# Optimization experiments

Hardware: AMD Instinct MI355X
Metric: run time of the kernel (lower is better)

## Reference

```python
import itertools
import jax, jax.numpy as jnp
import numpy as np

# ---- config (mirrors args) ----
BS = 8; C = 20              # 4 + num_sem_categories
FH, FW = 480, 640           # frame height/width
DU = 2                      # du_scale
NSC = 16                    # num_sem_categories
RES = 5; ZRES = 5           # xy / z map resolution (cm)
MAP_CM = 4800 // 2          # map_size_cm // global_downscaling
VR = 100                    # vision_range
HFOV = 79.0
MAXH = int(200 / ZRES); MINH = int(-40 / ZRES)   # 40, -8
AGENT_H = 0.88 * 100.0
CAT_T, EXP_T, MAP_T = 5.0, 1.0, 1.0
STAIR_R = 30
DEG = 57.29577951308232
M = MAP_CM // RES           # 480 local map cells

CAM_XC = (FW - 1.) / 2.
CAM_ZC = (FH - 1.) / 2.
CAM_F = (FW / 2.) / np.tan(np.deg2rad(HFOV / 2.))
SHIFT_X = VR * RES // 2     # shift_loc theta = pi/2 -> identity rotation, +x only

def _circle_mask(r):
    size = 2 * r
    ii, jj = np.meshgrid(np.arange(size), np.arange(size), indexing='ij')
    return (((ii + 0.5 - size // 2) ** 2 + (jj + 0.5 - size // 2) ** 2) <= r ** 2).astype(np.float32)

CIRCLE = jnp.asarray(_circle_mask(STAIR_R))

def splat_feat_nd(init_grid, feat, coords):
    # init_grid [B,F,d0,d1,d2], feat [B,F,N], coords [B,3,N] in [-1,1]
    B, nF = init_grid.shape[:2]
    gd = init_grid.shape[2:]
    grid_flat = init_grid.reshape(B, nF, -1)
    pos_dim, wts_dim = [], []
    for d in range(3):
        pos = coords[:, d, :] * gd[d] / 2 + gd[d] / 2
        pd, wd = [], []
        for ix in (0, 1):
            pos_ix = jnp.floor(pos) + ix
            safe = ((pos_ix > 0) & (pos_ix < gd[d])).astype(pos.dtype)
            wd.append((1 - jnp.abs(pos - pos_ix)) * safe)
            pd.append(pos_ix * safe)
        pos_dim.append(pd); wts_dim.append(wd)
    idxs, vals = [], []
    for ix_d in itertools.product((0, 1), repeat=3):  # 8 trilinear corners
        index = jnp.zeros_like(pos_dim[0][0])
        wts = jnp.ones_like(wts_dim[0][0])
        for d in range(3):
            index = index * gd[d] + pos_dim[d][ix_d[d]]
            wts = wts * wts_dim[d][ix_d[d]]
        idxs.append(index.astype(jnp.int32))
        vals.append(feat * wts[:, None, :])
    idx = jnp.concatenate(idxs, -1)          # [B, 8N]
    val = jnp.concatenate(vals, -1)          # [B, F, 8N]
    grid_flat = jax.vmap(lambda g, i, v: g.at[:, i].add(v))(grid_flat, idx, val)
    return jnp.round(grid_flat).reshape(init_grid.shape)

def affine_grid(theta, H, W):
    # F.affine_grid, align_corners=False (torch default)
    xs = (jnp.arange(W, dtype=theta.dtype) + 0.5) * 2 / W - 1
    ys = (jnp.arange(H, dtype=theta.dtype) + 0.5) * 2 / H - 1
    gy, gx = jnp.meshgrid(ys, xs, indexing='ij')
    base = jnp.stack([gx, gy, jnp.ones_like(gx)], -1)   # [H,W,3]
    return jnp.einsum('bij,hwj->bhwi', theta, base)     # [B,H,W,2]

def grid_sample(img, grid):
    # bilinear, zero padding, align_corners=True
    B, C_, H, W = img.shape
    gx = (grid[..., 0] + 1.) * (W - 1) / 2.
    gy = (grid[..., 1] + 1.) * (H - 1) / 2.
    x0 = jnp.floor(gx); y0 = jnp.floor(gy)
    def gather(ix, iy):
        valid = ((ix >= 0) & (ix < W) & (iy >= 0) & (iy < H)).astype(img.dtype)
        ic = jnp.clip(ix, 0, W - 1).astype(jnp.int32)
        jc = jnp.clip(iy, 0, H - 1).astype(jnp.int32)
        v = jax.vmap(lambda im, yy, xx: im[:, yy, xx])(img, jc, ic)  # [B,C,H,W]
        return v * valid[:, None]
    wx1 = gx - x0; wx0 = 1 - wx1; wy1 = gy - y0; wy0 = 1 - wy1
    return (gather(x0, y0) * (wx0 * wy0)[:, None]
            + gather(x0 + 1, y0) * (wx1 * wy0)[:, None]
            + gather(x0, y0 + 1) * (wx0 * wy1)[:, None]
            + gather(x0 + 1, y0 + 1) * (wx1 * wy1)[:, None])

def maxpool3(x):
    return jax.lax.reduce_window(x, -jnp.inf, jax.lax.max,
                                 (1, 1, 3, 3), (1, 1, 1, 1),
                                 [(0, 0), (0, 0), (1, 1), (1, 1)])

def _forward(obs, pose_obs, maps_last, poses_last, eve_angle):
    bs, c, h, w = obs.shape
    hs, ws = h // DU, w // DU
    depth = obs[:, 3, ::DU, ::DU]
    # point cloud from depth (du.get_point_cloud_from_z_t)
    xg = jnp.arange(0, w, DU, dtype=obs.dtype)[None, None, :]
    zg = (h - 1 - jnp.arange(0, h, DU, dtype=obs.dtype))[None, :, None]
    X = (xg - CAM_XC) * depth / CAM_F
    Z = (zg - CAM_ZC) * depth / CAM_F
    # camera elevation rotation about x-axis (per-env eve_angle) + sensor height
    th = jnp.deg2rad(eve_angle)[:, None, None]
    ct, st = jnp.cos(th), jnp.sin(th)
    Yr = ct * depth - st * Z
    Zr = st * depth + ct * Z + AGENT_H
    Xs = X + SHIFT_X
    # normalize to [-1,1] voxel coords
    cx = (Xs / RES - VR // 2) / VR * 2.0
    cy = (Yr / RES - VR // 2) / VR * 2.0
    cz = (Zr / ZRES - (MAXH + MINH) // 2) / (MAXH - MINH) * 2.0
    coords = jnp.stack([cx.reshape(bs, -1), cy.reshape(bs, -1), cz.reshape(bs, -1)], 1)
    sem = obs[:, 4:].reshape(bs, c - 4, hs, DU, ws, DU).mean((3, 5))  # AvgPool2d(du)
    feat = jnp.concatenate([jnp.ones((bs, 1, hs * ws), obs.dtype),
                            sem.reshape(bs, c - 4, hs * ws)], 1)
    init_grid = jnp.zeros((bs, 1 + NSC, VR, VR, MAXH - MINH), obs.dtype)
    voxels = splat_feat_nd(init_grid, feat, coords).transpose(0, 1, 3, 2, 4)
    min_z = int(25 / ZRES - MINH)
    max_z = int((AGENT_H + 50) / ZRES - MINH)
    mid_z = int(AGENT_H / ZRES - MINH)
    ah_proj = voxels[..., min_z:max_z].sum(-1)
    stair_proj = voxels[..., mid_z - 5:mid_z].sum(-1)
    all_proj = voxels.sum(-1)
    fp_map = jnp.clip(ah_proj[:, 0:1] / MAP_T, 0., 1.)
    fp_stair = jnp.clip(stair_proj[:, 0:1] / MAP_T, 0., 1.)
    fp_exp = jnp.clip(all_proj[:, 0:1] / EXP_T, 0., 1.)
    x1 = M // 2 - VR // 2; x2 = x1 + VR; y1 = M // 2; y2 = y1 + VR
    agent_view = jnp.zeros((bs, c, M, M), obs.dtype)
    agent_view = agent_view.at[:, 0:1, y1:y2, x1:x2].set(fp_map)
    agent_view = agent_view.at[:, 1:2, y1:y2, x1:x2].set(fp_exp)
    agent_view = agent_view.at[:, 4:, y1:y2, x1:x2].set(jnp.clip(ah_proj[:, 1:] / CAT_T, 0., 1.))
    agent_view_stair = jax.lax.stop_gradient(agent_view).at[:, 0:1, y1:y2, x1:x2].set(fp_stair)
    # pose integration (get_new_pose_batch)
    tr = poses_last[:, 2] / DEG
    ny = poses_last[:, 1] + pose_obs[:, 0] * jnp.sin(tr) + pose_obs[:, 1] * jnp.cos(tr)
    nx = poses_last[:, 0] + pose_obs[:, 0] * jnp.cos(tr) - pose_obs[:, 1] * jnp.sin(tr)
    no = poses_last[:, 2] + pose_obs[:, 2] * DEG
    no = jnp.fmod(no - 180.0, 360.0) + 180.0
    no = jnp.fmod(no + 180.0, 360.0) - 180.0
    current_poses = jnp.stack([nx, ny, no], 1)
    cp = jax.lax.stop_gradient(current_poses)  # st_pose = clone().detach()
    half = M // 2
    st_xy = -(cp[:, :2] * 100.0 / RES - half) / half
    st_t = (90.0 - cp[:, 2]) * np.pi / 180.0
    c_, s_ = jnp.cos(st_t), jnp.sin(st_t)
    zeros = jnp.zeros_like(c_); ones = jnp.ones_like(c_)
    theta1 = jnp.stack([jnp.stack([c_, -s_, zeros], 1), jnp.stack([s_, c_, zeros], 1)], 1)
    theta2 = jnp.stack([jnp.stack([ones, zeros, st_xy[:, 0]], 1),
                        jnp.stack([zeros, ones, st_xy[:, 1]], 1)], 1)
    rot_grid = affine_grid(theta1, M, M)
    trans_grid = affine_grid(theta2, M, M)
    translated = grid_sample(grid_sample(agent_view, rot_grid), trans_grid)
    diff = translated[:, 1:2] - maxpool3(translated[:, 0:1])
    diff = jnp.where(diff > 0.8, 1.0, 0.0).astype(obs.dtype)
    maps2 = jnp.maximum(maps_last, translated)
    m0 = (eve_angle == 0)[:, None, None, None] & (diff == 1.0)
    map_pred = maps2.at[:, 0:1].set(jnp.where(m0, 0.0, maps2[:, 0:1]))
    # stair map
    translated_stair = grid_sample(grid_sample(agent_view_stair, rot_grid), trans_grid)
    s_y = jnp.clip((cp[0, 1] * 100 / 5).astype(jnp.int32), STAIR_R, M - STAIR_R - 1)
    s_x = jnp.clip((cp[0, 0] * 100 / 5).astype(jnp.int32), STAIR_R, M - STAIR_R - 1)
    full_mask = jax.lax.dynamic_update_slice(jnp.zeros((M, M), obs.dtype), CIRCLE.astype(obs.dtype),
                                             (s_y - STAIR_R, s_x - STAIR_R))
    translated_stair = translated_stair.at[0, 0:2].multiply(full_mask)
    diff_s = translated_stair[:, 1:2] - translated_stair[:, 0:1]
    diff_s = jnp.where(diff_s > 0.8, 1.0, 0.0).astype(obs.dtype)
    maps3 = jnp.maximum(maps_last, translated_stair)
    m0s = (eve_angle == 0)[:, None, None, None] & (diff_s == 1.0)
    map_pred_stair = maps3.at[:, 0:1].set(jnp.where(m0s, 0.0, maps3[:, 0:1]))
    return translated, map_pred, map_pred_stair, current_poses

def setup_inputs() -> dict:
    key = jax.random.key(0)
    k1, k2, k3, k4, k5 = jax.random.split(key, 5)
    obs = jax.random.uniform(k1, (BS, C, FH, FW), jnp.float32)
    depth = 50.0 + 350.0 * jax.random.uniform(k2, (BS, FH, FW), jnp.float32)  # depth in cm
    obs = obs.at[:, 3].set(depth)
    pose_obs = jax.random.normal(k3, (BS, 3), jnp.float32) * jnp.array([0.1, 0.05, 0.02], jnp.float32)
    maps_last = jax.random.uniform(k4, (BS, C, M, M), jnp.float32)
    poses_last = (jnp.tile(jnp.array([12.0, 12.0, 0.0], jnp.float32), (BS, 1))
                  + jax.random.normal(k5, (BS, 3), jnp.float32) * jnp.array([0.5, 0.5, 30.0], jnp.float32))
    eve_angle = jnp.array([0., 0., -30., 0., 30., 0., 0., 0.], jnp.float32)
    return {'obs': obs, 'pose_obs': pose_obs, 'maps_last': maps_last,
            'poses_last': poses_last, 'eve_angle': eve_angle}

def reference(obs, pose_obs, maps_last, poses_last, eve_angle):
    return _forward(obs, pose_obs, maps_last, poses_last, eve_angle)
```

## Files before the change

### kernel.cpp

```cpp
#include <hip/hip_runtime.h>
#include <cmath>

#define NBS 8
#define NC 20
#define NFH 480
#define NFW 640
#define NHS 240
#define NWS 320
#define NM 480
#define NPIX (NM * NM)
#define NPIXELS (NBS * NHS * NWS)
#define PPB (NHS * NWS)
#define YW 20

constexpr long long T_OFF    = 0LL;
constexpr long long P_OFF    = 36864000LL;
constexpr long long S_OFF    = 73728000LL;
constexpr long long POSE_OFF = 110592000LL;

constexpr long long SMAP_O = 0LL;
constexpr long long PAR_O  = SMAP_O + 1600000LL;
constexpr long long REC_O  = PAR_O + 64LL;
constexpr long long EPOS_O = REC_O + 2457600LL;
constexpr long long ESEM_O = EPOS_O + 2457600LL;
constexpr long long CNT_O  = ESEM_O + 9830400LL;
constexpr long long OFF_O  = CNT_O + 80000LL;
constexpr long long CUR_O  = OFF_O + 80000LL;
constexpr long long SCR_END = CUR_O + 80000LL;

__device__ __forceinline__ float clamp01(float x) {
    return fminf(fmaxf(x, 0.0f), 1.0f);
}

__device__ __forceinline__ void project_px(const float* __restrict__ ob, float ev,
                                           float camf, int iy, int ix,
                                           float& posx, float& posy, float& posz,
                                           bool& alive, bool& semz) {
    float depth = ob[(3LL * NFH + 2 * iy) * NFW + 2 * ix];
    float th = ev * 0.017453292519943295f;
    float ct = cosf(th), st = sinf(th);
    float X = ((float)(2 * ix) - 319.5f) * depth / camf;
    float Z = ((float)(479 - 2 * iy) - 239.5f) * depth / camf;
    float Yr = ct * depth - st * Z;
    float Zr = st * depth + ct * Z + 88.0f;
    float Xs = X + 250.0f;
    float cx = ((Xs / 5.0f) - 50.0f) / 100.0f * 2.0f;
    float cy = ((Yr / 5.0f) - 50.0f) / 100.0f * 2.0f;
    float cz = ((Zr / 5.0f) - 16.0f) / 48.0f * 2.0f;
    posx = (cx * 100.0f) / 2.0f + 50.0f;
    posy = (cy * 100.0f) / 2.0f + 50.0f;
    posz = (cz * 48.0f) / 2.0f + 24.0f;
    alive = (posx > 0.0f) && (posx < 100.0f) &&
            (posy > 0.0f) && (posy < 100.0f) &&
            (posz > 0.0f) && (posz < 48.0f);
    semz = (posz > 12.0f) && (posz < 35.0f);
}

__global__ void k_pose(const float* __restrict__ pose_obs,
                       const float* __restrict__ poses_last,
                       float* __restrict__ pose_out,
                       float* __restrict__ par) {
    int b = threadIdx.x;
    if (b >= NBS) return;
    const float DEGf = 57.29577951308232f;
    float tr = poses_last[b * 3 + 2] / DEGf;
    float s_tr = sinf(tr), c_tr = cosf(tr);
    float ny = poses_last[b * 3 + 1] + pose_obs[b * 3 + 0] * s_tr + pose_obs[b * 3 + 1] * c_tr;
    float nx = poses_last[b * 3 + 0] + pose_obs[b * 3 + 0] * c_tr - pose_obs[b * 3 + 1] * s_tr;
    float no = poses_last[b * 3 + 2] + pose_obs[b * 3 + 2] * DEGf;
    no = fmodf(no - 180.0f, 360.0f) + 180.0f;
    no = fmodf(no + 180.0f, 360.0f) - 180.0f;
    pose_out[b * 3 + 0] = nx;
    pose_out[b * 3 + 1] = ny;
    pose_out[b * 3 + 2] = no;
    float stx = -((nx * 100.0f) / 5.0f - 240.0f) / 240.0f;
    float sty = -((ny * 100.0f) / 5.0f - 240.0f) / 240.0f;
    float stt = ((90.0f - no) * 3.14159265358979323846f) / 180.0f;
    par[b * 4 + 0] = cosf(stt);
    par[b * 4 + 1] = sinf(stt);
    par[b * 4 + 2] = stx;
    par[b * 4 + 3] = sty;
    if (b == 0) {
        int sy = (int)((ny * 100.0f) / 5.0f);
        int sx = (int)((nx * 100.0f) / 5.0f);
        sy = min(max(sy, 30), NM - 31);
        sx = min(max(sx, 30), NM - 31);
        par[32] = (float)sy;
        par[33] = (float)sx;
    }
}

__global__ void k_count(const float* __restrict__ obs,
                        const float* __restrict__ eve, float camf,
                        unsigned int* __restrict__ counts,
                        float4* __restrict__ rec) {
    int tid = blockIdx.x * blockDim.x + threadIdx.x;
    if (tid >= NPIXELS) return;
    int b = tid / PPB;
    int p = tid % PPB;
    int iy = p / NWS, ix = p % NWS;
    const float* ob = obs + (long long)b * NC * NFH * NFW;
    float posx, posy, posz;
    bool alive, semz;
    project_px(ob, eve[b], camf, iy, ix, posx, posy, posz, alive, semz);
    float flag = alive ? (semz ? 2.0f : 1.0f) : 0.0f;
    rec[tid] = make_float4(posx, posy, posz, flag);
    if (!alive) return;
    int fx = (int)floorf(posx);
    int fy = (int)floorf(posy);
    atomicAdd(&counts[b * 10000 + fx * 100 + fy], 1u);
}

__global__ void __launch_bounds__(1024) k_scan(const unsigned int* __restrict__ counts,
                                               unsigned int* __restrict__ offs,
                                               unsigned int* __restrict__ curs) {
    int b = blockIdx.x;
    int t = threadIdx.x;
    int lane = t & 63, wid = t >> 6;
    const unsigned int* cb = counts + b * 10000;
    unsigned int base_i = (unsigned int)t * 10u;
    unsigned int v[10];
    unsigned int s = 0;
#pragma unroll
    for (int k = 0; k < 10; ++k) {
        unsigned int i = base_i + (unsigned int)k;
        unsigned int x = (i < 10000u) ? cb[i] : 0u;
        v[k] = s;
        s += x;
    }
    unsigned int incl = s;
#pragma unroll
    for (int d = 1; d < 64; d <<= 1) {
        unsigned int u = __shfl_up(incl, d);
        if (lane >= d) incl += u;
    }
    __shared__ unsigned int wtot[16];
    __shared__ unsigned int wexc[16];
    if (lane == 63) wtot[wid] = incl;
    __syncthreads();
    if (t == 0) {
        unsigned int a = 0;
        for (int i = 0; i < 16; ++i) { wexc[i] = a; a += wtot[i]; }
    }
    __syncthreads();
    unsigned int tbase = wexc[wid] + (incl - s);
#pragma unroll
    for (int k = 0; k < 10; ++k) {
        unsigned int i = base_i + (unsigned int)k;
        if (i < 10000u) {
            unsigned int e = tbase + v[k];
            offs[b * 10000 + i] = e;
            curs[b * 10000 + i] = e;
        }
    }
}

__global__ void k_fill(const float* __restrict__ obs,
                       const float4* __restrict__ rec,
                       unsigned int* __restrict__ curs,
                       float4* __restrict__ epos,
                       float4* __restrict__ esem4) {
    int tid = blockIdx.x * blockDim.x + threadIdx.x;
    if (tid >= NPIXELS) return;
    float4 r = rec[tid];
    if (r.w == 0.0f) return;
    int b = tid / PPB;
    int p = tid % PPB;
    int iy = p / NWS, ix = p % NWS;
    int fx = (int)floorf(r.x);
    int fy = (int)floorf(r.y);
    unsigned int slot = atomicAdd(&curs[b * 10000 + fx * 100 + fy], 1u);
    long long gslot = (long long)b * PPB + slot;
    epos[gslot] = make_float4(r.x, r.y, r.z, 0.0f);
    if (r.w == 2.0f) {
        const float* ob = obs + (long long)b * NC * NFH * NFW;
        float sem[16];
#pragma unroll
        for (int k = 0; k < 16; ++k) {
            const float* q = ob + ((long long)(4 + k) * NFH + 2 * iy) * NFW + 2 * ix;
            sem[k] = (q[0] + q[1] + q[NFW] + q[NFW + 1]) * 0.25f;
        }
#pragma unroll
        for (int g = 0; g < 4; ++g)
            esem4[gslot * 4 + g] =
                make_float4(sem[4 * g], sem[4 * g + 1], sem[4 * g + 2], sem[4 * g + 3]);
    }
}

__global__ void __launch_bounds__(256) k_accum(const float4* __restrict__ epos,
                                               const float4* __restrict__ esem4,
                                               const unsigned int* __restrict__ counts,
                                               const unsigned int* __restrict__ offs,
                                               float* __restrict__ smap) {
    int blk = blockIdx.x;
    int b = blk / 500;
    int r = blk % 500;
    int x = r / 5;
    int y0 = (r % 5) * YW;
    __shared__ float acc[YW][400];
    int tid = threadIdx.x;
    for (int i2 = tid; i2 < YW * 400; i2 += 256) (&acc[0][0])[i2] = 0.0f;
    __syncthreads();
    if (x >= 1) {
        int byLo = max(y0 - 1, 0);
        int byHi = min(y0 + YW - 1, 99);
        int base = b * 10000;
        int s0i = base + (x - 1) * 100 + byLo;
        int e0i = base + (x - 1) * 100 + byHi;
        int s1i = base + x * 100 + byLo;
        int e1i = base + x * 100 + byHi;
        unsigned int st0 = offs[s0i];
        unsigned int n0 = offs[e0i] + counts[e0i] - st0;
        unsigned int st1 = offs[s1i];
        unsigned int n1 = offs[e1i] + counts[e1i] - st1;
        unsigned int E = n0 + n1;
        const float4* pb = epos + (long long)b * PPB;
        const float4* sb = esem4 + (long long)b * PPB * 4;
        float xf = (float)x;
        for (unsigned int t = tid; t < E; t += 256) {
            unsigned int idx = (t < n0) ? (st0 + t) : (st1 + (t - n0));
            float4 e = pb[idx];
            float wx = 1.0f - fabsf(e.x - xf);
            if (wx <= 0.0f) continue;
            float posy = e.y, posz = e.z;
            int fyi = (int)floorf(posy);
            float fz = floorf(posz);
            bool zsem = (posz > 12.0f) && (posz < 35.0f);
            float sem[16];
            if (zsem) {
#pragma unroll
                for (int g = 0; g < 4; ++g) {
                    float4 s4 = sb[(long long)idx * 4 + g];
                    sem[4 * g + 0] = s4.x; sem[4 * g + 1] = s4.y;
                    sem[4 * g + 2] = s4.z; sem[4 * g + 3] = s4.w;
                }
            }
#pragma unroll
            for (int dy2 = 0; dy2 < 2; ++dy2) {
                int cy = fyi + dy2;
                if (cy < 1 || cy >= 100 || cy < y0 || cy >= y0 + YW) continue;
                float w2 = wx * (1.0f - fabsf(posy - (float)cy));
                if (w2 <= 0.0f) continue;
                float* A = acc[cy - y0];
#pragma unroll
                for (int d = 0; d < 2; ++d) {
                    float zf = fz + (float)d;
                    int z = (int)zf;
                    if (z < 1 || z > 47) continue;
                    float w = w2 * (1.0f - fabsf(posz - zf));
                    if (w == 0.0f) continue;
                    atomicAdd(&A[z], w);
                    if (z >= 13 && z < 35) {
                        float* ap = A + 48 + (z - 13) * 16;
#pragma unroll
                        for (int k = 0; k < 16; ++k)
                            atomicAdd(ap + k, sem[k] * w);
                    }
                }
            }
        }
    }
    __syncthreads();
    float* smb = smap + (long long)b * 200000;
    for (int o = tid; o < YW * 20; o += 256) {
        int ly = o / 20, ch = o % 20;
        int cy = y0 + ly;
        const float* A = acc[ly];
        float s = 0.0f;
        if (ch == 0) {
            for (int z = 13; z < 35; ++z) s += rintf(A[z]);
            s = clamp01(s);
        } else if (ch == 1) {
            for (int z = 0; z < 48; ++z) s += rintf(A[z]);
            s = clamp01(s);
        } else if (ch == 2) {
            for (int z = 20; z < 25; ++z) s += rintf(A[z]);
            s = clamp01(s);
        } else if (ch < 19) {
            int k = ch - 3;
            for (int z = 13; z < 35; ++z) s += rintf(A[48 + (z - 13) * 16 + k]);
            s = clamp01(s / 5.0f);
        }
        smb[(long long)(cy * 100 + x) * 20 + ch] = s;
    }
}

template<bool FULL>
__device__ __forceinline__ void eval_pix(int i, int j, const float* __restrict__ smb,
                                         float c, float s, float stx, float sty,
                                         float& a0, float& a1, float& as_, float* cat) {
    a0 = 0.0f; a1 = 0.0f; as_ = 0.0f;
    float gx = (((float)j + 0.5f) * 2.0f) / 480.0f - 1.0f;
    float gy = (((float)i + 0.5f) * 2.0f) / 480.0f - 1.0f;
    float px = ((gx + stx) + 1.0f) * 479.0f / 2.0f;
    float py = ((gy + sty) + 1.0f) * 479.0f / 2.0f;
    float x0 = floorf(px), y0 = floorf(py);
    float wx1 = px - x0, wx0 = 1.0f - wx1;
    float wy1 = py - y0, wy0 = 1.0f - wy1;
#pragma unroll
    for (int t = 0; t < 4; ++t) {
        int ox = t & 1, oy = t >> 1;
        float xo = x0 + (float)ox, yo = y0 + (float)oy;
        if (!(xo >= 0.0f && xo < 480.0f && yo >= 0.0f && yo < 480.0f)) continue;
        float wo = (ox ? wx1 : wx0) * (oy ? wy1 : wy0);
        int ixo = (int)xo, iyo = (int)yo;
        float gx2 = (((float)ixo + 0.5f) * 2.0f) / 480.0f - 1.0f;
        float gy2 = (((float)iyo + 0.5f) * 2.0f) / 480.0f - 1.0f;
        float rx = c * gx2 - s * gy2;
        float ry = s * gx2 + c * gy2;
        float qx = (rx + 1.0f) * 479.0f / 2.0f;
        float qy = (ry + 1.0f) * 479.0f / 2.0f;
        float xq0 = floorf(qx), yq0 = floorf(qy);
        float u1 = qx - xq0, u0 = 1.0f - u1;
        float v1 = qy - yq0, v0 = 1.0f - v1;
#pragma unroll
        for (int t2 = 0; t2 < 4; ++t2) {
            int ax = t2 & 1, ay = t2 >> 1;
            float xa = xq0 + (float)ax, ya = yq0 + (float)ay;
            if (xa >= 190.0f && xa < 290.0f && ya >= 240.0f && ya < 340.0f) {
                float w = wo * ((ax ? u1 : u0) * (ay ? v1 : v0));
                if (w != 0.0f) {
                    int o = ((int)ya - 240) * 100 + ((int)xa - 190);
                    const float* bp = smb + (long long)o * 20;
                    if constexpr (FULL) {
                        const float4* b4 = (const float4*)bp;
                        float4 v0_ = b4[0], v1_ = b4[1], v2_ = b4[2], v3_ = b4[3], v4_ = b4[4];
                        a0 += w * v0_.x; a1 += w * v0_.y; as_ += w * v0_.z;
                        cat[0]  += w * v0_.w;
                        cat[1]  += w * v1_.x; cat[2]  += w * v1_.y;
                        cat[3]  += w * v1_.z; cat[4]  += w * v1_.w;
                        cat[5]  += w * v2_.x; cat[6]  += w * v2_.y;
                        cat[7]  += w * v2_.z; cat[8]  += w * v2_.w;
                        cat[9]  += w * v3_.x; cat[10] += w * v3_.y;
                        cat[11] += w * v3_.z; cat[12] += w * v3_.w;
                        cat[13] += w * v4_.x; cat[14] += w * v4_.y;
                        cat[15] += w * v4_.z;
                    } else {
                        a0 += w * bp[0];
                    }
                }
            }
        }
    }
}

template<bool WRITEP>
__global__ void __launch_bounds__(256) k_translate(float* __restrict__ outp,
                                                   const float* __restrict__ smap,
                                                   const float* __restrict__ par,
                                                   const float* __restrict__ maps_last,
                                                   const float* __restrict__ eve) {
    int tid = blockIdx.x * blockDim.x + threadIdx.x;
    int b = tid / NPIX;
    int ij = tid % NPIX;
    int i = ij / NM, j = ij % NM;
    float c = par[b * 4 + 0], s = par[b * 4 + 1];
    float stx = par[b * 4 + 2], sty = par[b * 4 + 3];
    const float* smb = smap + (long long)b * 200000;
    const float* ml = maps_last + (long long)b * NC * NPIX;
    long long obase = (long long)b * NC * NPIX + ij;
    bool eve0 = (eve[b] == 0.0f);

    float gxp = (((float)j + 0.5f) * 2.0f) / 480.0f - 1.0f + stx;
    float gyp = (((float)i + 0.5f) * 2.0f) / 480.0f - 1.0f + sty;
    float rxp = c * gxp - s * gyp, ryp = s * gxp + c * gyp;
    float qxc = (rxp + 1.0f) * 239.5f, qyc = (ryp + 1.0f) * 239.5f;
    bool near_ = (qxc > 184.0f) && (qxc < 296.0f) && (qyc > 234.0f) && (qyc < 346.0f);

    float a0 = 0.0f, a1 = 0.0f, as_ = 0.0f;
    float cat[16];
#pragma unroll
    for (int k = 0; k < 16; ++k) cat[k] = 0.0f;
    float mp = 0.0f;
    if (near_) {
        eval_pix<true>(i, j, smb, c, s, stx, sty, a0, a1, as_, cat);
        if constexpr (WRITEP) {
            mp = -INFINITY;
#pragma unroll
            for (int di = -1; di <= 1; ++di) {
                int ii = i + di;
                if (ii < 0 || ii >= NM) continue;
#pragma unroll
                for (int dj = -1; dj <= 1; ++dj) {
                    int jj = j + dj;
                    if (jj < 0 || jj >= NM) continue;
                    float b0, b1, b2;
                    if (di == 0 && dj == 0) b0 = a0;
                    else eval_pix<false>(ii, jj, smb, c, s, stx, sty, b0, b1, b2, nullptr);
                    mp = fmaxf(mp, b0);
                }
            }
        }
    }

    float mlv[NC];
#pragma unroll
    for (int ch = 0; ch < NC; ++ch) mlv[ch] = ml[(long long)ch * NPIX + ij];

    float* To = outp + T_OFF;
    To[obase] = a0;
    To[obase + (long long)NPIX] = a1;
    To[obase + 2LL * NPIX] = 0.0f;
    To[obase + 3LL * NPIX] = 0.0f;
#pragma unroll
    for (int k = 0; k < 16; ++k) To[obase + (long long)(4 + k) * NPIX] = cat[k];

    float ts0 = as_, t1s = a1;
    if (b == 0) {
        float dy = (float)i - par[32] + 0.5f;
        float dx = (float)j - par[33] + 0.5f;
        float mask = (dy * dy + dx * dx <= 900.0f) ? 1.0f : 0.0f;
        ts0 *= mask;
        t1s *= mask;
    }
    bool flagS = (t1s - ts0) > 0.8f;
    float* So = outp + S_OFF;
#pragma unroll
    for (int ch = 0; ch < NC; ++ch) {
        float tch = (ch == 0) ? ts0 : (ch == 1) ? t1s
                  : (ch < 4) ? 0.0f : cat[ch - 4];
        float m3 = fmaxf(mlv[ch], tch);
        So[obase + (long long)ch * NPIX] = (ch == 0 && eve0 && flagS) ? 0.0f : m3;
    }

    if constexpr (WRITEP) {
        bool flagP = (a1 - mp) > 0.8f;
        float* Po = outp + P_OFF;
#pragma unroll
        for (int ch = 0; ch < NC; ++ch) {
            float tch = (ch == 0) ? a0 : (ch == 1) ? a1
                      : (ch < 4) ? 0.0f : cat[ch - 4];
            float m2 = fmaxf(mlv[ch], tch);
            Po[obase + (long long)ch * NPIX] = (ch == 0 && eve0 && flagP) ? 0.0f : m2;
        }
    }
}

__global__ void k_pred(const float* __restrict__ T, const float* __restrict__ maps_last,
                       const float* __restrict__ eve, float* __restrict__ outP) {
    int tid = blockIdx.x * blockDim.x + threadIdx.x;
    if (tid >= NBS * NPIX) return;
    int b = tid / NPIX;
    int ij = tid % NPIX;
    int i = ij / NM, j = ij % NM;
    const float* Tb = T + (long long)b * NC * NPIX;
    float mp = -INFINITY;
#pragma unroll
    for (int di = -1; di <= 1; ++di) {
        int ii = i + di;
        if (ii < 0 || ii >= NM) continue;
#pragma unroll
        for (int dj = -1; dj <= 1; ++dj) {
            int jj = j + dj;
            if (jj < 0 || jj >= NM) continue;
            mp = fmaxf(mp, Tb[(long long)ii * NM + jj]);
        }
    }
    float t1 = Tb[(long long)NPIX + ij];
    bool flag = (t1 - mp) > 0.8f;
    bool eve0 = (eve[b] == 0.0f);
    const float* ml = maps_last + (long long)b * NC * NPIX;
    long long obase = (long long)b * NC * NPIX + ij;
#pragma unroll
    for (int ch = 0; ch < NC; ++ch) {
        float m2 = fmaxf(ml[(long long)ch * NPIX + ij], Tb[(long long)ch * NPIX + ij]);
        outP[obase + (long long)ch * NPIX] = (ch == 0 && eve0 && flag) ? 0.0f : m2;
    }
}

extern "C" void kernel_launch(void* const* d_in, const int* in_sizes, int n_in,
                              void* d_out, int out_size, void* d_ws, size_t ws_size,
                              hipStream_t stream) {
    const float* obs = (const float*)d_in[0];
    const float* pose_obs = (const float*)d_in[1];
    const float* maps_last = (const float*)d_in[2];
    const float* poses_last = (const float*)d_in[3];
    const float* eve = (const float*)d_in[4];
    float* outp = (float*)d_out;

    float camf = (float)(320.0 / tan(39.5 * M_PI / 180.0));

    bool useWS = (d_ws != nullptr) && (ws_size >= (size_t)SCR_END * 4);
    float* scr = useWS ? (float*)d_ws : (outp + P_OFF);

    float* smapp = scr + SMAP_O;
    float* par   = scr + PAR_O;
    float4* rec   = (float4*)(scr + REC_O);
    float4* epos  = (float4*)(scr + EPOS_O);
    float4* esem4 = (float4*)(scr + ESEM_O);
    unsigned int* counts = (unsigned int*)(scr + CNT_O);
    unsigned int* offs2  = (unsigned int*)(scr + OFF_O);
    unsigned int* curs   = (unsigned int*)(scr + CUR_O);

    hipMemsetAsync(counts, 0, 80000 * sizeof(unsigned int), stream);

    k_pose<<<1, 64, 0, stream>>>(pose_obs, poses_last, outp + POSE_OFF, par);

    k_count<<<NPIXELS / 256, 256, 0, stream>>>(obs, eve, camf, counts, rec);

    k_scan<<<NBS, 1024, 0, stream>>>(counts, offs2, curs);

    k_fill<<<NPIXELS / 256, 256, 0, stream>>>(obs, rec, curs, epos, esem4);

    k_accum<<<NBS * 500, 256, 0, stream>>>(epos, esem4, counts, offs2, smapp);

    if (useWS) {
        k_translate<true><<<(NBS * NPIX) / 256, 256, 0, stream>>>(outp, smapp, par,
                                                                  maps_last, eve);
    } else {
        k_translate<false><<<(NBS * NPIX) / 256, 256, 0, stream>>>(outp, smapp, par,
                                                                   maps_last, eve);
        k_pred<<<(NBS * NPIX) / 256, 256, 0, stream>>>(outp + T_OFF, maps_last, eve,
                                                       outp + P_OFF);
    }
}
```

Before: 1.129 ms.

## Map one wavefront per map column in accumulation and rotate semantic channels

The accumulation kernel now gives each 64-lane wavefront a single (x,y) map column, with four columns per block. Before, each 256-thread block handled a strip of 20 y-cells and scanned the points of a wider range of cells. Each wave reads only the four neighbouring bins, and the per-point y-range checks go away. The fill kernel stores the 16 semantic values rotated by the slot index, and the accumulator adds them into a 32-wide doubled buffer at a rotated offset, then folds the two halves back together. The rotation is meant to spread shared-memory atomic bank conflicts across lanes, at the cost of more shared memory per column and a small extra reduction. Launch count grows to one wave per column, so load balance depends on how many points land in each bin.

After: 1.088 ms. 1.04x faster.

```diff
diff --git a/kernel.cpp b/kernel.cpp
--- a/kernel.cpp
+++ b/kernel.cpp
@@ -11,7 +11,8 @@
 #define NPIX (NM * NM)
 #define NPIXELS (NBS * NHS * NWS)
 #define PPB (NHS * NWS)
-#define YW 20
+#define CPB 4
+#define CWORDS 752
 
 constexpr long long T_OFF    = 0LL;
 constexpr long long P_OFF    = 36864000LL;
@@ -174,16 +175,18 @@
     epos[gslot] = make_float4(r.x, r.y, r.z, 0.0f);
     if (r.w == 2.0f) {
         const float* ob = obs + (long long)b * NC * NFH * NFW;
-        float sem[16];
+        int rrot = (int)(slot & 15u);
+        float srot[16];
 #pragma unroll
         for (int k = 0; k < 16; ++k) {
-            const float* q = ob + ((long long)(4 + k) * NFH + 2 * iy) * NFW + 2 * ix;
-            sem[k] = (q[0] + q[1] + q[NFW] + q[NFW + 1]) * 0.25f;
+            int kk = (k + rrot) & 15;
+            const float* q = ob + ((long long)(4 + kk) * NFH + 2 * iy) * NFW + 2 * ix;
+            srot[k] = (q[0] + q[1] + q[NFW] + q[NFW + 1]) * 0.25f;
         }
 #pragma unroll
         for (int g = 0; g < 4; ++g)
             esem4[gslot * 4 + g] =
-                make_float4(sem[4 * g], sem[4 * g + 1], sem[4 * g + 2], sem[4 * g + 3]);
+                make_float4(srot[4 * g], srot[4 * g + 1], srot[4 * g + 2], srot[4 * g + 3]);
     }
 }
 
@@ -192,96 +195,87 @@
                                                const unsigned int* __restrict__ counts,
                                                const unsigned int* __restrict__ offs,
                                                float* __restrict__ smap) {
-    int blk = blockIdx.x;
-    int b = blk / 500;
-    int r = blk % 500;
-    int x = r / 5;
-    int y0 = (r % 5) * YW;
-    __shared__ float acc[YW][400];
-    int tid = threadIdx.x;
-    for (int i2 = tid; i2 < YW * 400; i2 += 256) (&acc[0][0])[i2] = 0.0f;
+    int wid = threadIdx.x >> 6, lane = threadIdx.x & 63;
+    int col = blockIdx.x * CPB + wid;
+    int b = col / 10000;
+    int xy = col % 10000;
+    int x = xy / 100, y = xy % 100;
+    __shared__ float acc[CPB][CWORDS];
+    float* A = acc[wid];
+    for (int i = lane; i < CWORDS; i += 64) A[i] = 0.0f;
     __syncthreads();
-    if (x >= 1) {
-        int byLo = max(y0 - 1, 0);
-        int byHi = min(y0 + YW - 1, 99);
+    if (x >= 1 && y >= 1) {
         int base = b * 10000;
-        int s0i = base + (x - 1) * 100 + byLo;
-        int e0i = base + (x - 1) * 100 + byHi;
-        int s1i = base + x * 100 + byLo;
-        int e1i = base + x * 100 + byHi;
-        unsigned int st0 = offs[s0i];
-        unsigned int n0 = offs[e0i] + counts[e0i] - st0;
-        unsigned int st1 = offs[s1i];
-        unsigned int n1 = offs[e1i] + counts[e1i] - st1;
+        int b00 = base + (x - 1) * 100 + (y - 1);
+        int b01 = base + (x - 1) * 100 + y;
+        int b10 = base + x * 100 + (y - 1);
+        int b11 = base + x * 100 + y;
+        unsigned int s0 = offs[b00];
+        unsigned int n0 = offs[b01] + counts[b01] - s0;
+        unsigned int s1 = offs[b10];
+        unsigned int n1 = offs[b11] + counts[b11] - s1;
         unsigned int E = n0 + n1;
         const float4* pb = epos + (long long)b * PPB;
         const float4* sb = esem4 + (long long)b * PPB * 4;
-        float xf = (float)x;
-        for (unsigned int t = tid; t < E; t += 256) {
-            unsigned int idx = (t < n0) ? (st0 + t) : (st1 + (t - n0));
+        float fx_ = (float)x, fy_ = (float)y;
+        for (unsigned int t = lane; t < E; t += 64) {
+            unsigned int idx = (t < n0) ? (s0 + t) : (s1 + (t - n0));
             float4 e = pb[idx];
-            float wx = 1.0f - fabsf(e.x - xf);
-            if (wx <= 0.0f) continue;
-            float posy = e.y, posz = e.z;
-            int fyi = (int)floorf(posy);
+            float wx = 1.0f - fabsf(e.x - fx_);
+            float wy = 1.0f - fabsf(e.y - fy_);
+            float wxy = wx * wy;
+            if (wxy <= 0.0f) continue;
+            float posz = e.z;
             float fz = floorf(posz);
             bool zsem = (posz > 12.0f) && (posz < 35.0f);
-            float sem[16];
+            float sr[16];
             if (zsem) {
-#pragma unroll
-                for (int g = 0; g < 4; ++g) {
-                    float4 s4 = sb[(long long)idx * 4 + g];
-                    sem[4 * g + 0] = s4.x; sem[4 * g + 1] = s4.y;
-                    sem[4 * g + 2] = s4.z; sem[4 * g + 3] = s4.w;
+                const float4* sp = sb + (long long)idx * 4;
+                float4 q0 = sp[0], q1 = sp[1], q2 = sp[2], q3 = sp[3];
+                sr[0] = q0.x;  sr[1] = q0.y;  sr[2] = q0.z;  sr[3] = q0.w;
+                sr[4] = q1.x;  sr[5] = q1.y;  sr[6] = q1.z;  sr[7] = q1.w;
+                sr[8] = q2.x;  sr[9] = q2.y;  sr[10] = q2.z; sr[11] = q2.w;
+                sr[12] = q3.x; sr[13] = q3.y; sr[14] = q3.z; sr[15] = q3.w;
+            }
+            int rbase = (int)(idx & 15u);
+#pragma unroll
+            for (int d = 0; d < 2; ++d) {
+                float zf = fz + (float)d;
+                int z = (int)zf;
+                if (z < 1 || z > 47) continue;
+                float w = wxy * (1.0f - fabsf(posz - zf));
+                if (w == 0.0f) continue;
+                atomicAdd(&A[z], w);
+                if (z >= 13 && z < 35) {
+                    float* ap = A + 48 + (z - 13) * 32 + rbase;
+#pragma unroll
+                    for (int s2 = 0; s2 < 16; ++s2)
+                        atomicAdd(ap + s2, sr[s2] * w);
                 }
             }
-#pragma unroll
-            for (int dy2 = 0; dy2 < 2; ++dy2) {
-                int cy = fyi + dy2;
-                if (cy < 1 || cy >= 100 || cy < y0 || cy >= y0 + YW) continue;
-                float w2 = wx * (1.0f - fabsf(posy - (float)cy));
-                if (w2 <= 0.0f) continue;
-                float* A = acc[cy - y0];
-#pragma unroll
-                for (int d = 0; d < 2; ++d) {
-                    float zf = fz + (float)d;
-                    int z = (int)zf;
-                    if (z < 1 || z > 47) continue;
-                    float w = w2 * (1.0f - fabsf(posz - zf));
-                    if (w == 0.0f) continue;
-                    atomicAdd(&A[z], w);
-                    if (z >= 13 && z < 35) {
-                        float* ap = A + 48 + (z - 13) * 16;
-#pragma unroll
-                        for (int k = 0; k < 16; ++k)
-                            atomicAdd(ap + k, sem[k] * w);
-                    }
-                }
-            }
         }
     }
     __syncthreads();
     float* smb = smap + (long long)b * 200000;
-    for (int o = tid; o < YW * 20; o += 256) {
-        int ly = o / 20, ch = o % 20;
-        int cy = y0 + ly;
-        const float* A = acc[ly];
+    int ij = y * 100 + x;
+    if (lane < 20) {
         float s = 0.0f;
-        if (ch == 0) {
+        if (lane == 0) {
             for (int z = 13; z < 35; ++z) s += rintf(A[z]);
             s = clamp01(s);
-        } else if (ch == 1) {
+        } else if (lane == 1) {
             for (int z = 0; z < 48; ++z) s += rintf(A[z]);
             s = clamp01(s);
-        } else if (ch == 2) {
+        } else if (lane == 2) {
             for (int z = 20; z < 25; ++z) s += rintf(A[z]);
             s = clamp01(s);
-        } else if (ch < 19) {
-            int k = ch - 3;
-            for (int z = 13; z < 35; ++z) s += rintf(A[48 + (z - 13) * 16 + k]);
+        } else if (lane < 19) {
+            int k = lane - 3;
+            for (int zi = 0; zi < 22; ++zi)
+                s += rintf(A[48 + zi * 32 + k] + A[48 + zi * 32 + 16 + k]);
             s = clamp01(s / 5.0f);
         }
-        smb[(long long)(cy * 100 + x) * 20 + ch] = s;
+        smb[(long long)ij * 20 + lane] = s;
     }
 }
 
@@ -502,7 +496,8 @@
 
     k_fill<<<NPIXELS / 256, 256, 0, stream>>>(obs, rec, curs, epos, esem4);
 
-    k_accum<<<NBS * 500, 256, 0, stream>>>(epos, esem4, counts, offs2, smapp);
+    k_accum<<<(NBS * 10000) / CPB, 256, 0, stream>>>(epos, esem4, counts, offs2,
+                                                     smapp);
 
     if (useWS) {
         k_translate<true><<<(NBS * NPIX) / 256, 256, 0, stream>>>(outp, smapp, par,
```
